# Kernel tuning notes

Measured on AMD Instinct MI355X. Metric: run time of the kernel, lower is better.

The kernel has to match this reference:

```python
import jax, jax.numpy as jnp
import numpy as np

B, C, S, HID = 64, 512, 28, 256  # batch, channels, spatial size, LSTM hidden


def _param(k, shape):
    return jax.random.normal(k, shape, jnp.float32) * 0.05


def setup_inputs() -> dict:
    key = jax.random.key(0)
    ks = jax.random.split(key, 19)
    inp = {"x": jax.random.normal(ks[0], (B, C, S, S), jnp.float32)}
    # vertical bidirectional LSTM (input C, hidden HID), torch gate order i,f,g,o
    inp["v_wih_f"] = _param(ks[1], (4 * HID, C))
    inp["v_whh_f"] = _param(ks[2], (4 * HID, HID))
    inp["v_b_f"] = _param(ks[3], (4 * HID,))
    inp["v_wih_b"] = _param(ks[4], (4 * HID, C))
    inp["v_whh_b"] = _param(ks[5], (4 * HID, HID))
    inp["v_b_b"] = _param(ks[6], (4 * HID,))
    # horizontal bidirectional LSTM (input 2*HID=512, hidden HID)
    inp["h_wih_f"] = _param(ks[7], (4 * HID, 2 * HID))
    inp["h_whh_f"] = _param(ks[8], (4 * HID, HID))
    inp["h_b_f"] = _param(ks[9], (4 * HID,))
    inp["h_wih_b"] = _param(ks[10], (4 * HID, 2 * HID))
    inp["h_whh_b"] = _param(ks[11], (4 * HID, HID))
    inp["h_b_b"] = _param(ks[12], (4 * HID,))
    # 1x1 conv 512 -> 100 (10x10 attention kernel logits)
    inp["conv_w"] = _param(ks[13], (100, 2 * HID))
    inp["conv_b"] = _param(ks[14], (100,))
    return inp


def _lstm_scan(xs, wih, whh, b):
    # xs: [T, N, D] -> h sequence [T, N, HID]
    hdim = whh.shape[1]
    def step(carry, xt):
        h, c = carry
        gates = xt @ wih.T + h @ whh.T + b  # [N, 4H]
        i, f, g, o = jnp.split(gates, 4, axis=-1)
        c = jax.nn.sigmoid(f) * c + jax.nn.sigmoid(i) * jnp.tanh(g)
        h = jax.nn.sigmoid(o) * jnp.tanh(c)
        return (h, c), h
    n = xs.shape[1]
    z = jnp.zeros((n, hdim), xs.dtype)
    _, hs = jax.lax.scan(step, (z, z), xs)
    return hs


def _bilstm(x, wf, uf, bf, wb, ub, bb):
    # x: [N, T, D] -> [N, T, 2*HID]
    xs = jnp.swapaxes(x, 0, 1)
    hf = _lstm_scan(xs, wf, uf, bf)
    hb = _lstm_scan(xs[::-1], wb, ub, bb)[::-1]
    return jnp.swapaxes(jnp.concatenate([hf, hb], axis=-1), 0, 1)


def reference(x, v_wih_f, v_whh_f, v_b_f, v_wih_b, v_whh_b, v_b_b,
              h_wih_f, h_whh_f, h_b_f, h_wih_b, h_whh_b, h_b_b,
              conv_w, conv_b):
    b, c, s, _ = x.shape
    xt = jnp.transpose(x, (0, 3, 2, 1))            # [B, W, H, C]
    # vertical LSTM: seq over W, batched over (B, H)
    v_in = jnp.transpose(xt, (0, 2, 1, 3)).reshape(b * s, s, c)
    v_out = _bilstm(v_in, v_wih_f, v_whh_f, v_b_f, v_wih_b, v_whh_b, v_b_b)
    v_out = jnp.transpose(v_out.reshape(b, s, s, 2 * HID), (0, 2, 1, 3))  # [B, W, H, 512]
    # horizontal LSTM: seq over H, batched over (B, W)
    h_in = v_out.reshape(b * s, s, 2 * HID)
    h_out = _bilstm(h_in, h_wih_f, h_whh_f, h_b_f, h_wih_b, h_whh_b, h_b_b)
    feat = jnp.transpose(h_out.reshape(b, s, s, 2 * HID), (0, 3, 2, 1))  # [B, 512, H, W]
    # 1x1 conv -> [B, 100, H, W], softmax over 100 kernel entries
    kern = jnp.einsum('bfhw,of->bohw', feat, conv_w) + conv_b[None, :, None, None]
    kern = jax.nn.softmax(kern, axis=1)
    # faithful to torch: C-order reshape [B,100,H,W] -> (B*H*W, 100) kernels
    w = kern.reshape(b, s * s, 100)
    # grouped dilated conv3d == weighted sum over dilation-3 sampled 10x10 grid
    x_s = x[:, :, ::3, ::3].reshape(b, c, 100)     # [B, C, 100]
    out = jnp.einsum('bpk,bck->bpc', w, x_s)       # [B, H*W, C]
    return out.reshape(b, c, s, s)                 # faithful C-order reshape
```

## Files before the change

kernel.cpp:

```cpp
#include <hip/hip_runtime.h>
#include <hip/hip_bf16.h>
#include <stdint.h>

typedef __hip_bfloat16 bf16_t;
typedef __attribute__((ext_vector_type(8))) short short8;
typedef __attribute__((ext_vector_type(4))) float f32x4;
typedef __attribute__((ext_vector_type(4))) unsigned int u32x4;
typedef unsigned long long ull;

#define MFMA16(a, b, c) __builtin_amdgcn_mfma_f32_16x16x32_bf16(a, b, c, 0, 0, 0)

#define NROW 50176
#define NBATCH 1792

__device__ __forceinline__ void g2l16(const void* g, void* l) {
  __builtin_amdgcn_global_load_lds(
      (const __attribute__((address_space(1))) unsigned int*)g,
      (__attribute__((address_space(3))) unsigned int*)l, 16, 0, 0);
}
__device__ __forceinline__ float sigm(float x) { return 1.0f / (1.0f + __expf(-x)); }
__device__ __forceinline__ float tanh_(float x) { return 2.0f / (1.0f + __expf(-2.0f * x)) - 1.0f; }
__device__ __forceinline__ void stc(bf16_t* p, float v) { *p = __float2bfloat16(v); }
__device__ __forceinline__ void stc(float* p, float v) { *p = v; }
__device__ __forceinline__ float bf2f(unsigned short u) {
  return __uint_as_float((unsigned int)u << 16);
}

struct CvtArgs {
  const float* src[8];
  bf16_t* dst[8];
  int n[8];
};
__global__ void cvt_all(CvtArgs a) {
  int arr = blockIdx.y;
  int i = blockIdx.x * 256 + threadIdx.x;
  if (i < a.n[arr]) a.dst[arr][i] = __float2bfloat16(a.src[arr][i]);
}

__global__ void transpose_x(const float* __restrict__ x, bf16_t* __restrict__ Xin,
                            bf16_t* __restrict__ xs) {
  int c0 = blockIdx.x * 128, h = blockIdx.y, b = blockIdx.z;
  __shared__ __align__(16) short tile[128 * 29];
  const float* xb = x + ((size_t)b * 512 + c0) * 784 + h * 28;
  for (int e = threadIdx.x; e < 128 * 28; e += 256) {
    int cc = e / 28, w = e - cc * 28;
    tile[cc * 29 + w] = __bfloat16_as_short(__float2bfloat16(xb[(size_t)cc * 784 + w]));
  }
  __syncthreads();
  size_t orow0 = (size_t)(b * 28 + h) * 28;
  short* os = (short*)Xin;
  for (int e = threadIdx.x; e < 28 * 128; e += 256) {
    int w = e >> 7, cc = e & 127;
    int c = c0 + cc;
    os[(size_t)(c >> 5) * NROW * 32 + (orow0 + w) * 32 + (c & 31)] = tile[cc * 29 + w];
  }
  short* xss = (short*)xs;
  if (h % 3 == 0) {
    int kh = h / 3;
    for (int e = threadIdx.x; e < 1280; e += 256) {
      int cc = e / 10, kw = e - cc * 10;
      xss[((size_t)(b * 512) + c0 + cc) * 128 + kh * 10 + kw] = tile[cc * 29 + 3 * kw];
    }
  }
  if (h == 0) {
    for (int e = threadIdx.x; e < 128 * 28; e += 256) {
      int cc = e / 28, kp = e - cc * 28;
      xss[((size_t)(b * 512) + c0 + cc) * 128 + 100 + kp] = 0;
    }
  }
}

__global__ void pad_conv(const float* __restrict__ cw, const float* __restrict__ cb,
                         bf16_t* __restrict__ cwp, float* __restrict__ cbp,
                         unsigned int* __restrict__ bar) {
  int r = blockIdx.x;
  if (r == 0)
    for (int i = threadIdx.x; i < 7168; i += 128) bar[i] = 0;
  for (int i = threadIdx.x; i < 512; i += 128)
    cwp[r * 512 + i] = __float2bfloat16((r < 100) ? cw[r * 512 + i] : 0.0f);
  if (r == 0) cbp[threadIdx.x] = (threadIdx.x < 100) ? cb[threadIdx.x] : 0.0f;
}

template <typename CT, bool CPERM>
__global__ __launch_bounds__(256) void gemm_bt(
    const bf16_t* __restrict__ A, const bf16_t* __restrict__ B0,
    const bf16_t* __restrict__ B1, const float* __restrict__ bias0,
    const float* __restrict__ bias1, CT* __restrict__ C, int M, int N, int K) {
  __shared__ __align__(16) short As[2][128 * 32];
  __shared__ __align__(16) short Bs[2][128 * 32];
  int tid = threadIdx.x;
  int L = blockIdx.x;
  int xc = L & 7, j = L >> 3;
  int mp = xc * 49 + (j % 49);
  int nb = j / 49;
  int bm0 = mp * 128, bn0 = nb * 128;
  int lrow = tid >> 2, lseg = tid & 3;
  const char* Ag = (const char*)A + ((size_t)(bm0 + lrow) * 32 + lseg * 8) * 2;
  size_t Aadv = (size_t)M * 64;
  const float* biasp;
  const char *Bg1, *Bg2;
  int js = 0;
  if (CPERM) {
    int dir = nb >> 3;
    js = nb & 7;
    const bf16_t* Bsel = dir ? B1 : B0;
    biasp = dir ? bias1 : bias0;
    int br1 = (lrow >> 5) * 256 + js * 32 + (lrow & 31);
    int br2 = ((lrow + 64) >> 5) * 256 + js * 32 + (lrow & 31);
    Bg1 = (const char*)(Bsel + (size_t)br1 * K) + lseg * 16;
    Bg2 = (const char*)(Bsel + (size_t)br2 * K) + lseg * 16;
  } else {
    biasp = bias0 + bn0;
    Bg1 = (const char*)(B0 + (size_t)(bn0 + lrow) * K) + lseg * 16;
    Bg2 = Bg1 + (size_t)64 * K * 2;
  }
  int w = tid >> 6, l = tid & 63, lm = l & 15, lq = l >> 4;
  int wm = w & 1, wn = w >> 1;
  f32x4 acc[4][4] = {};
  for (int k0 = 0; k0 < K; k0 += 64) {
#pragma unroll
    for (int p = 0; p < 2; p++) {
      g2l16(Ag, (char*)As[p] + tid * 16);
      g2l16(Ag + 4096, (char*)As[p] + 4096 + tid * 16);
      g2l16(Bg1, (char*)Bs[p] + tid * 16);
      g2l16(Bg2, (char*)Bs[p] + 4096 + tid * 16);
      Ag += Aadv; Bg1 += 64; Bg2 += 64;
    }
    __syncthreads();
#pragma unroll
    for (int p = 0; p < 2; p++) {
      short8 afr[4], bfr[4];
#pragma unroll
      for (int i = 0; i < 4; i++) {
        afr[i] = *(const short8*)&As[p][(wm * 64 + i * 16 + lm) * 32 + lq * 8];
        bfr[i] = *(const short8*)&Bs[p][(wn * 64 + i * 16 + lm) * 32 + lq * 8];
      }
#pragma unroll
      for (int mi = 0; mi < 4; mi++)
#pragma unroll
        for (int ni = 0; ni < 4; ni++) acc[mi][ni] = MFMA16(afr[mi], bfr[ni], acc[mi][ni]);
    }
    __syncthreads();
  }
  float bv[4];
#pragma unroll
  for (int ni = 0; ni < 4; ni++) {
    int cb = wn * 64 + ni * 16 + lm;
    bv[ni] = CPERM ? biasp[(cb >> 5) * 256 + js * 32 + (cb & 31)] : biasp[cb];
  }
#pragma unroll
  for (int mi = 0; mi < 4; mi++)
#pragma unroll
    for (int ni = 0; ni < 4; ni++) {
      int col = bn0 + wn * 64 + ni * 16 + lm;
#pragma unroll
      for (int r = 0; r < 4; r++) {
        size_t row = bm0 + wm * 64 + mi * 16 + lq * 4 + r;
        stc(&C[row * N + col], acc[mi][ni][r] + bv[ni]);
      }
    }
}

__global__ __launch_bounds__(256) void conv_softmax(
    const bf16_t* __restrict__ A, const bf16_t* __restrict__ B0,
    const float* __restrict__ bias, bf16_t* __restrict__ Wscr, int M, int K) {
  __shared__ __align__(16) short As[2][128 * 32];
  __shared__ __align__(16) short Bs[2][128 * 32];
  __shared__ float part[2][128];
  int tid = threadIdx.x;
  int bm0 = blockIdx.x * 128;
  int lrow = tid >> 2, lseg = tid & 3;
  const char* Ag = (const char*)A + ((size_t)(bm0 + lrow) * 32 + lseg * 8) * 2;
  size_t Aadv = (size_t)M * 64;
  const char* Bg1 = (const char*)(B0 + (size_t)lrow * K) + lseg * 16;
  const char* Bg2 = Bg1 + (size_t)64 * K * 2;
  int w = tid >> 6, l = tid & 63, lm = l & 15, lq = l >> 4;
  int wm = w & 1, wn = w >> 1;
  f32x4 acc[4][4] = {};
  for (int k0 = 0; k0 < K; k0 += 64) {
#pragma unroll
    for (int p = 0; p < 2; p++) {
      g2l16(Ag, (char*)As[p] + tid * 16);
      g2l16(Ag + 4096, (char*)As[p] + 4096 + tid * 16);
      g2l16(Bg1, (char*)Bs[p] + tid * 16);
      g2l16(Bg2, (char*)Bs[p] + 4096 + tid * 16);
      Ag += Aadv; Bg1 += 64; Bg2 += 64;
    }
    __syncthreads();
#pragma unroll
    for (int p = 0; p < 2; p++) {
      short8 afr[4], bfr[4];
#pragma unroll
      for (int i = 0; i < 4; i++) {
        afr[i] = *(const short8*)&As[p][(wm * 64 + i * 16 + lm) * 32 + lq * 8];
        bfr[i] = *(const short8*)&Bs[p][(wn * 64 + i * 16 + lm) * 32 + lq * 8];
      }
#pragma unroll
      for (int mi = 0; mi < 4; mi++)
#pragma unroll
        for (int ni = 0; ni < 4; ni++) acc[mi][ni] = MFMA16(afr[mi], bfr[ni], acc[mi][ni]);
    }
    __syncthreads();
  }
  float bv[4];
  bool vld[4];
#pragma unroll
  for (int ni = 0; ni < 4; ni++) {
    int col = wn * 64 + ni * 16 + lm;
    bv[ni] = bias[col];
    vld[ni] = (col < 100);
  }
  float pmax[4][4];
#pragma unroll
  for (int mi = 0; mi < 4; mi++)
#pragma unroll
    for (int r = 0; r < 4; r++) {
      float m = -1e30f;
#pragma unroll
      for (int ni = 0; ni < 4; ni++)
        if (vld[ni]) m = fmaxf(m, acc[mi][ni][r] + bv[ni]);
      pmax[mi][r] = m;
    }
#pragma unroll
  for (int mask = 1; mask <= 8; mask <<= 1)
#pragma unroll
    for (int mi = 0; mi < 4; mi++)
#pragma unroll
      for (int r = 0; r < 4; r++) pmax[mi][r] = fmaxf(pmax[mi][r], __shfl_xor(pmax[mi][r], mask));
  if (lm == 0)
#pragma unroll
    for (int mi = 0; mi < 4; mi++)
#pragma unroll
      for (int r = 0; r < 4; r++) part[wn][wm * 64 + mi * 16 + lq * 4 + r] = pmax[mi][r];
  __syncthreads();
  float fm[4][4];
#pragma unroll
  for (int mi = 0; mi < 4; mi++)
#pragma unroll
    for (int r = 0; r < 4; r++)
      fm[mi][r] = fmaxf(pmax[mi][r], part[wn ^ 1][wm * 64 + mi * 16 + lq * 4 + r]);
  __syncthreads();
  float ev[4][4][4];
  float ps[4][4];
#pragma unroll
  for (int mi = 0; mi < 4; mi++)
#pragma unroll
    for (int r = 0; r < 4; r++) {
      float s = 0.0f;
#pragma unroll
      for (int ni = 0; ni < 4; ni++) {
        float e = vld[ni] ? __expf(acc[mi][ni][r] + bv[ni] - fm[mi][r]) : 0.0f;
        ev[mi][ni][r] = e;
        s += e;
      }
      ps[mi][r] = s;
    }
#pragma unroll
  for (int mask = 1; mask <= 8; mask <<= 1)
#pragma unroll
    for (int mi = 0; mi < 4; mi++)
#pragma unroll
      for (int r = 0; r < 4; r++) ps[mi][r] += __shfl_xor(ps[mi][r], mask);
  if (lm == 0)
#pragma unroll
    for (int mi = 0; mi < 4; mi++)
#pragma unroll
      for (int r = 0; r < 4; r++) part[wn][wm * 64 + mi * 16 + lq * 4 + r] = ps[mi][r];
  __syncthreads();
#pragma unroll
  for (int mi = 0; mi < 4; mi++)
#pragma unroll
    for (int r = 0; r < 4; r++) {
      float inv =
          1.0f / (ps[mi][r] + part[wn ^ 1][wm * 64 + mi * 16 + lq * 4 + r]);
      int grow = bm0 + wm * 64 + mi * 16 + lq * 4 + r;
      int b = grow / 784, q = grow - b * 784;
      size_t base = (size_t)b * 784 * 128;
#pragma unroll
      for (int ni = 0; ni < 4; ni++) {
        int col = wn * 64 + ni * 16 + lm;
        if (col < 100) {
          int mm = col * 784 + q;
          Wscr[base + (size_t)(mm / 100) * 128 + (mm % 100)] =
              __float2bfloat16(ev[mi][ni][r] * inv);
        }
      }
    }
}

__global__ __launch_bounds__(256, 2) void lstm_scan(
    const bf16_t* __restrict__ G, const bf16_t* __restrict__ whh_f,
    const bf16_t* __restrict__ whh_b, bf16_t* __restrict__ hA,
    bf16_t* __restrict__ hB, bf16_t* __restrict__ outb,
    unsigned int* __restrict__ bar) {
  int dir = blockIdx.y;
  int js = blockIdx.x & 7;
  int rg = blockIdx.x >> 3;
  int tid = threadIdx.x, w = tid >> 6, l = tid & 63, lm = l & 15, lq = l >> 4;
  const short* whh = (const short*)(dir ? whh_b : whh_f);
  __shared__ __align__(16) short Ws[128 * 256];
  __shared__ __align__(16) short ht[64 * 40];
#pragma unroll
  for (int i = 0; i < 16; i++) {
    int segid = i * 256 + tid;
    int row = segid >> 5, seg = segid & 31;
    int gate = row >> 5, jj = row & 31;
    short8 v = *(const short8*)&whh[((size_t)(gate * 256 + js * 32 + jj)) * 256 + seg * 8];
    *(short8*)&Ws[row * 256 + ((seg ^ (row & 7)) * 8)] = v;
  }
  __syncthreads();
  unsigned int* cnt = bar + (((dir * 28 + rg) << 2) + w) * 16;
  int r0 = rg * 64 + w * 16;
  size_t dbase = (size_t)dir * 458752;
  const unsigned short* Gb = (const unsigned short*)G + (size_t)dir * 1024 + js * 128;
  float creg[2][4] = {};
  unsigned short gvs[2][4][4];
  auto load_gvs = [&](int tt) {
#pragma unroll
    for (int nj = 0; nj < 2; nj++)
#pragma unroll
      for (int r = 0; r < 4; r++) {
        int bi = r0 + lq * 4 + r;
        const unsigned short* gp = Gb + ((size_t)bi * 28 + tt) * 2048 + nj * 16 + lm;
#pragma unroll
        for (int gate = 0; gate < 4; gate++) gvs[nj][gate][r] = gp[gate * 32];
      }
  };
  load_gvs(dir ? 27 : 0);
  int srow = w * 16 + (l >> 2), sseg = l & 3;
  int sbi = rg * 64 + srow;
  int sbb = sbi / 28, srr = sbi - sbb * 28;
#pragma unroll 1
  for (int s = 0; s < 28; s++) {
    int t = dir ? 27 - s : s;
    f32x4 acc[4][2] = {};
    if (s > 0) {
      unsigned int tgt = 8u * (unsigned)s;
      while (__hip_atomic_load(cnt, __ATOMIC_RELAXED, __HIP_MEMORY_SCOPE_AGENT) < tgt)
        __builtin_amdgcn_s_sleep(1);
      const ull* hrp = (const ull*)((s & 1) ? hA : hB);
      ull hq[8][2];
#pragma unroll
      for (int kk = 0; kk < 8; kk++) {
        size_t off = dbase + (size_t)kk * 57344 + (size_t)(r0 + lm) * 32 + lq * 8;
        hq[kk][0] =
            __hip_atomic_load(hrp + (off >> 2), __ATOMIC_RELAXED, __HIP_MEMORY_SCOPE_AGENT);
        hq[kk][1] = __hip_atomic_load(hrp + (off >> 2) + 1, __ATOMIC_RELAXED,
                                      __HIP_MEMORY_SCOPE_AGENT);
      }
#pragma unroll
      for (int kk = 0; kk < 8; kk++) {
        short8 a;
        ((ull*)&a)[0] = hq[kk][0];
        ((ull*)&a)[1] = hq[kk][1];
        int bseg = ((kk * 4 + lq) ^ (lm & 7)) * 8;
#pragma unroll
        for (int gate = 0; gate < 4; gate++)
#pragma unroll
          for (int nj = 0; nj < 2; nj++) {
            short8 b = *(const short8*)&Ws[(gate * 32 + nj * 16 + lm) * 256 + bseg];
            acc[gate][nj] = MFMA16(a, b, acc[gate][nj]);
          }
      }
    }
#pragma unroll
    for (int nj = 0; nj < 2; nj++)
#pragma unroll
      for (int r = 0; r < 4; r++) {
        float gi = bf2f(gvs[nj][0][r]) + acc[0][nj][r];
        float gf = bf2f(gvs[nj][1][r]) + acc[1][nj][r];
        float gg = bf2f(gvs[nj][2][r]) + acc[2][nj][r];
        float go = bf2f(gvs[nj][3][r]) + acc[3][nj][r];
        float cn = sigm(gf) * creg[nj][r] + sigm(gi) * tanh_(gg);
        float hn = sigm(go) * tanh_(cn);
        creg[nj][r] = cn;
        ht[(w * 16 + lq * 4 + r) * 40 + nj * 16 + lm] =
            __bfloat16_as_short(__float2bfloat16(hn));
      }
    {
      u32x4 v = *(const u32x4*)&ht[srow * 40 + sseg * 8];
      ull* hwp = (ull*)((s & 1) ? hB : hA);
      size_t off = dbase + (size_t)js * 57344 + (size_t)sbi * 32 + sseg * 8;
      ull q0 = ((const ull*)&v)[0];
      ull q1 = ((const ull*)&v)[1];
      __hip_atomic_store(hwp + (off >> 2), q0, __ATOMIC_RELAXED, __HIP_MEMORY_SCOPE_AGENT);
      __hip_atomic_store(hwp + (off >> 2) + 1, q1, __ATOMIC_RELAXED,
                         __HIP_MEMORY_SCOPE_AGENT);
      short* ob = (short*)outb + (size_t)(dir * 8 + js) * NROW * 32;
      *(u32x4*)&ob[((size_t)sbb * 784 + (size_t)t * 28 + srr) * 32 + sseg * 8] = v;
    }
    if (s < 27) {
      asm volatile("s_waitcnt vmcnt(0)" ::: "memory");
      if (l == 0)
        __hip_atomic_fetch_add(cnt, 1u, __ATOMIC_RELAXED, __HIP_MEMORY_SCOPE_AGENT);
      load_gvs(dir ? 26 - s : s + 1);
    }
  }
}

__global__ __launch_bounds__(256) void final_gemm(const bf16_t* __restrict__ Wscr,
                                                  const bf16_t* __restrict__ xs,
                                                  float* __restrict__ outp) {
  int L = blockIdx.x;
  int xc = L & 7, j = L >> 3;
  int b = xc + 8 * (j / 28);
  int inner = j % 28;
  int m0 = (inner % 7) * 112, n0 = (inner / 7) * 128;
  int tid = threadIdx.x, w = tid >> 6, l = tid & 63, lm = l & 15, lq = l >> 4;
  const short* Ab = (const short*)Wscr + (size_t)b * 784 * 128;
  const short* Bb = (const short*)xs + (size_t)b * 512 * 128;
  f32x4 acc[7][2] = {};
#pragma unroll
  for (int kk = 0; kk < 4; kk++) {
    short8 b0 = *(const short8*)&Bb[(size_t)(n0 + w * 32 + lm) * 128 + kk * 32 + lq * 8];
    short8 b1 = *(const short8*)&Bb[(size_t)(n0 + w * 32 + 16 + lm) * 128 + kk * 32 + lq * 8];
#pragma unroll
    for (int mi = 0; mi < 7; mi++) {
      short8 a = *(const short8*)&Ab[(size_t)(m0 + mi * 16 + lm) * 128 + kk * 32 + lq * 8];
      acc[mi][0] = MFMA16(a, b0, acc[mi][0]);
      acc[mi][1] = MFMA16(a, b1, acc[mi][1]);
    }
  }
#pragma unroll
  for (int mi = 0; mi < 7; mi++)
#pragma unroll
    for (int ni = 0; ni < 2; ni++) {
      int c = n0 + w * 32 + ni * 16 + lm;
#pragma unroll
      for (int r = 0; r < 4; r++) {
        int p = m0 + mi * 16 + lq * 4 + r;
        outp[(size_t)b * 401408 + (size_t)p * 512 + c] = acc[mi][ni][r];
      }
    }
}

extern "C" void kernel_launch(void* const* d_in, const int* in_sizes, int n_in,
                              void* d_out, int out_size, void* d_ws, size_t ws_size,
                              hipStream_t stream) {
  const float* x = (const float*)d_in[0];
  const float* v_wih_f = (const float*)d_in[1];
  const float* v_whh_f = (const float*)d_in[2];
  const float* v_b_f = (const float*)d_in[3];
  const float* v_wih_b = (const float*)d_in[4];
  const float* v_whh_b = (const float*)d_in[5];
  const float* v_b_b = (const float*)d_in[6];
  const float* h_wih_f = (const float*)d_in[7];
  const float* h_whh_f = (const float*)d_in[8];
  const float* h_b_f = (const float*)d_in[9];
  const float* h_wih_b = (const float*)d_in[10];
  const float* h_whh_b = (const float*)d_in[11];
  const float* h_b_b = (const float*)d_in[12];
  const float* conv_w = (const float*)d_in[13];
  const float* conv_b = (const float*)d_in[14];

  char* ws = (char*)d_ws;
  bf16_t* Xin = (bf16_t*)(ws);
  bf16_t* Vout = (bf16_t*)(ws + 51380224);
  bf16_t* G = (bf16_t*)(ws + 102760448);
  bf16_t* Wscr = (bf16_t*)(ws + 128450560);
  bf16_t* xs = (bf16_t*)(ws + 308281344);
  bf16_t* cwp = (bf16_t*)(ws + 316669952);
  float* cbp = (float*)(ws + 316801024);
  bf16_t* hstate = (bf16_t*)(ws + 316801536);
  unsigned int* bar = (unsigned int*)(ws + 318636544);
  bf16_t* wvf = (bf16_t*)(ws + 322306560);
  bf16_t* wvb = (bf16_t*)(ws + 323355136);
  bf16_t* uvf = (bf16_t*)(ws + 324403712);
  bf16_t* uvb = (bf16_t*)(ws + 324928000);
  bf16_t* whf = (bf16_t*)(ws + 325452288);
  bf16_t* whb = (bf16_t*)(ws + 326500864);
  bf16_t* uhf = (bf16_t*)(ws + 327549440);
  bf16_t* uhb = (bf16_t*)(ws + 328073728);
  bf16_t* Hout = Xin;

  CvtArgs ca;
  ca.src[0] = v_wih_f; ca.dst[0] = wvf; ca.n[0] = 524288;
  ca.src[1] = v_wih_b; ca.dst[1] = wvb; ca.n[1] = 524288;
  ca.src[2] = v_whh_f; ca.dst[2] = uvf; ca.n[2] = 262144;
  ca.src[3] = v_whh_b; ca.dst[3] = uvb; ca.n[3] = 262144;
  ca.src[4] = h_wih_f; ca.dst[4] = whf; ca.n[4] = 524288;
  ca.src[5] = h_wih_b; ca.dst[5] = whb; ca.n[5] = 524288;
  ca.src[6] = h_whh_f; ca.dst[6] = uhf; ca.n[6] = 262144;
  ca.src[7] = h_whh_b; ca.dst[7] = uhb; ca.n[7] = 262144;
  cvt_all<<<dim3(2048, 8), 256, 0, stream>>>(ca);

  transpose_x<<<dim3(4, 28, 64), 256, 0, stream>>>(x, Xin, xs);
  pad_conv<<<dim3(128), 128, 0, stream>>>(conv_w, conv_b, cwp, cbp, bar);

  gemm_bt<bf16_t, true><<<dim3(6272), 256, 0, stream>>>(
      Xin, wvf, wvb, v_b_f, v_b_b, G, NROW, 2048, 512);
  lstm_scan<<<dim3(224, 2), 256, 0, stream>>>(G, uvf, uvb, hstate, Xin, Vout, bar);

  gemm_bt<bf16_t, true><<<dim3(6272), 256, 0, stream>>>(
      Vout, whf, whb, h_b_f, h_b_b, G, NROW, 2048, 512);
  lstm_scan<<<dim3(224, 2), 256, 0, stream>>>(G, uhf, uhb, hstate, Vout, Hout, bar + 3584);

  conv_softmax<<<dim3(392), 256, 0, stream>>>(Hout, cwp, cbp, Wscr, NROW, 512);
  final_gemm<<<dim3(1792), 256, 0, stream>>>(Wscr, xs, (float*)d_out);
}
```

Baseline: 969.8 us.

## Replace input-projection GEMM with 256x256-tile, 4-stage pipelined, swizzled-LDS kernel

Replaces the 128x128 double-buffered input-projection GEMM with a 512-thread kernel using 256x256 tiles and a 4-deep ring of LDS stages. Loads are issued three stages ahead with explicit vmcnt waits and one barrier per k-step. A XOR swizzle on LDS rows avoids bank conflicts, and the gate-permuted column mapping is kept. The aim is to raise data reuse per tile and overlap global loads with MFMA work. In exchange it uses 128KB of LDS per block, more registers for the accumulators, and fewer blocks (1568).

```diff
diff --git a/kernel.cpp b/kernel.cpp
--- a/kernel.cpp
+++ b/kernel.cpp
@@ -20,8 +20,6 @@
 }
 __device__ __forceinline__ float sigm(float x) { return 1.0f / (1.0f + __expf(-x)); }
 __device__ __forceinline__ float tanh_(float x) { return 2.0f / (1.0f + __expf(-2.0f * x)) - 1.0f; }
-__device__ __forceinline__ void stc(bf16_t* p, float v) { *p = __float2bfloat16(v); }
-__device__ __forceinline__ void stc(float* p, float v) { *p = v; }
 __device__ __forceinline__ float bf2f(unsigned short u) {
   return __uint_as_float((unsigned int)u << 16);
 }
@@ -81,82 +79,106 @@
   if (r == 0) cbp[threadIdx.x] = (threadIdx.x < 100) ? cb[threadIdx.x] : 0.0f;
 }
 
-template <typename CT, bool CPERM>
-__global__ __launch_bounds__(256) void gemm_bt(
+__global__ __launch_bounds__(512, 2) void gemm256(
     const bf16_t* __restrict__ A, const bf16_t* __restrict__ B0,
     const bf16_t* __restrict__ B1, const float* __restrict__ bias0,
-    const float* __restrict__ bias1, CT* __restrict__ C, int M, int N, int K) {
-  __shared__ __align__(16) short As[2][128 * 32];
-  __shared__ __align__(16) short Bs[2][128 * 32];
+    const float* __restrict__ bias1, bf16_t* __restrict__ C, int M) {
+  __shared__ __align__(16) short Asl[4][256 * 32];
+  __shared__ __align__(16) short Bsl[4][256 * 32];
   int tid = threadIdx.x;
-  int L = blockIdx.x;
-  int xc = L & 7, j = L >> 3;
-  int mp = xc * 49 + (j % 49);
-  int nb = j / 49;
-  int bm0 = mp * 128, bn0 = nb * 128;
-  int lrow = tid >> 2, lseg = tid & 3;
-  const char* Ag = (const char*)A + ((size_t)(bm0 + lrow) * 32 + lseg * 8) * 2;
+  int w = tid >> 6, l = tid & 63, lm = l & 15, lq = l >> 4;
+  int wm = w >> 2, wn = w & 3;
+  int bm0 = blockIdx.x * 256, bn0 = blockIdx.y * 256;
+  const char* ag[2];
+  const char* bg[2];
+#pragma unroll
+  for (int s = 0; s < 2; s++) {
+    int i = s * 512 + tid;
+    int row = i >> 2, sl = i & 3;
+    int sg = sl ^ ((row ^ (row >> 2)) & 3);
+    ag[s] = (const char*)A + ((size_t)(bm0 + row) * 32 + sg * 8) * 2;
+    int pc = bn0 + row;
+    int dir = pc >> 10, wc = pc & 1023;
+    int js = wc >> 7, loc = wc & 127;
+    int brow = (loc >> 5) * 256 + js * 32 + (loc & 31);
+    const bf16_t* Bsel = dir ? B1 : B0;
+    bg[s] = (const char*)(Bsel + (size_t)brow * 512) + sg * 16;
+  }
   size_t Aadv = (size_t)M * 64;
-  const float* biasp;
-  const char *Bg1, *Bg2;
-  int js = 0;
-  if (CPERM) {
-    int dir = nb >> 3;
-    js = nb & 7;
-    const bf16_t* Bsel = dir ? B1 : B0;
-    biasp = dir ? bias1 : bias0;
-    int br1 = (lrow >> 5) * 256 + js * 32 + (lrow & 31);
-    int br2 = ((lrow + 64) >> 5) * 256 + js * 32 + (lrow & 31);
-    Bg1 = (const char*)(Bsel + (size_t)br1 * K) + lseg * 16;
-    Bg2 = (const char*)(Bsel + (size_t)br2 * K) + lseg * 16;
-  } else {
-    biasp = bias0 + bn0;
-    Bg1 = (const char*)(B0 + (size_t)(bn0 + lrow) * K) + lseg * 16;
-    Bg2 = Bg1 + (size_t)64 * K * 2;
-  }
-  int w = tid >> 6, l = tid & 63, lm = l & 15, lq = l >> 4;
-  int wm = w & 1, wn = w >> 1;
-  f32x4 acc[4][4] = {};
-  for (int k0 = 0; k0 < K; k0 += 64) {
-#pragma unroll
-    for (int p = 0; p < 2; p++) {
-      g2l16(Ag, (char*)As[p] + tid * 16);
-      g2l16(Ag + 4096, (char*)As[p] + 4096 + tid * 16);
-      g2l16(Bg1, (char*)Bs[p] + tid * 16);
-      g2l16(Bg2, (char*)Bs[p] + 4096 + tid * 16);
-      Ag += Aadv; Bg1 += 64; Bg2 += 64;
-    }
-    __syncthreads();
-#pragma unroll
-    for (int p = 0; p < 2; p++) {
-      short8 afr[4], bfr[4];
-#pragma unroll
-      for (int i = 0; i < 4; i++) {
-        afr[i] = *(const short8*)&As[p][(wm * 64 + i * 16 + lm) * 32 + lq * 8];
-        bfr[i] = *(const short8*)&Bs[p][(wn * 64 + i * 16 + lm) * 32 + lq * 8];
-      }
-#pragma unroll
-      for (int mi = 0; mi < 4; mi++)
-#pragma unroll
-        for (int ni = 0; ni < 4; ni++) acc[mi][ni] = MFMA16(afr[mi], bfr[ni], acc[mi][ni]);
-    }
-    __syncthreads();
+  auto stage = [&](int t) {
+    int s4 = t & 3;
+#pragma unroll
+    for (int s = 0; s < 2; s++)
+      g2l16(ag[s] + (size_t)t * Aadv, (char*)&Asl[s4][0] + (s * 512 + w * 64) * 16);
+#pragma unroll
+    for (int s = 0; s < 2; s++)
+      g2l16(bg[s] + (size_t)t * 64, (char*)&Bsl[s4][0] + (s * 512 + w * 64) * 16);
+  };
+  int aoff[8], boff[4];
+#pragma unroll
+  for (int mi = 0; mi < 8; mi++) {
+    int row = wm * 128 + mi * 16 + lm;
+    aoff[mi] = (row * 4 + (lq ^ ((row ^ (row >> 2)) & 3))) * 8;
+  }
+#pragma unroll
+  for (int ni = 0; ni < 4; ni++) {
+    int row = wn * 64 + ni * 16 + lm;
+    boff[ni] = (row * 4 + (lq ^ ((row ^ (row >> 2)) & 3))) * 8;
+  }
+  f32x4 acc[8][4] = {};
+  stage(0);
+  stage(1);
+  stage(2);
+  asm volatile("s_waitcnt vmcnt(8)" ::: "memory");
+  __builtin_amdgcn_sched_barrier(0);
+  __builtin_amdgcn_s_barrier();
+  __builtin_amdgcn_sched_barrier(0);
+#pragma unroll 1
+  for (int t = 0; t < 16; t++) {
+    if (t < 13) stage(t + 3);
+    int s4 = t & 3;
+    const short* Ab = &Asl[s4][0];
+    const short* Bb = &Bsl[s4][0];
+    short8 bfr[4];
+#pragma unroll
+    for (int ni = 0; ni < 4; ni++) bfr[ni] = *(const short8*)&Bb[boff[ni]];
+    __builtin_amdgcn_s_setprio(1);
+#pragma unroll
+    for (int mi = 0; mi < 8; mi++) {
+      short8 afr = *(const short8*)&Ab[aoff[mi]];
+#pragma unroll
+      for (int ni = 0; ni < 4; ni++) acc[mi][ni] = MFMA16(afr, bfr[ni], acc[mi][ni]);
+    }
+    __builtin_amdgcn_s_setprio(0);
+    if (t < 13)
+      asm volatile("s_waitcnt vmcnt(8)" ::: "memory");
+    else if (t == 13)
+      asm volatile("s_waitcnt vmcnt(4)" ::: "memory");
+    else if (t == 14)
+      asm volatile("s_waitcnt vmcnt(0)" ::: "memory");
+    if (t < 15) {
+      __builtin_amdgcn_sched_barrier(0);
+      __builtin_amdgcn_s_barrier();
+      __builtin_amdgcn_sched_barrier(0);
+    }
   }
   float bv[4];
 #pragma unroll
   for (int ni = 0; ni < 4; ni++) {
-    int cb = wn * 64 + ni * 16 + lm;
-    bv[ni] = CPERM ? biasp[(cb >> 5) * 256 + js * 32 + (cb & 31)] : biasp[cb];
-  }
-#pragma unroll
-  for (int mi = 0; mi < 4; mi++)
+    int pc = bn0 + wn * 64 + ni * 16 + lm;
+    int dir = pc >> 10, wc = pc & 1023;
+    const float* bp = dir ? bias1 : bias0;
+    bv[ni] = bp[((wc & 127) >> 5) * 256 + (wc >> 7) * 32 + (wc & 31)];
+  }
+#pragma unroll
+  for (int mi = 0; mi < 8; mi++)
 #pragma unroll
     for (int ni = 0; ni < 4; ni++) {
       int col = bn0 + wn * 64 + ni * 16 + lm;
 #pragma unroll
       for (int r = 0; r < 4; r++) {
-        size_t row = bm0 + wm * 64 + mi * 16 + lq * 4 + r;
-        stc(&C[row * N + col], acc[mi][ni][r] + bv[ni]);
+        size_t row = bm0 + wm * 128 + mi * 16 + lq * 4 + r;
+        C[row * 2048 + col] = __float2bfloat16(acc[mi][ni][r] + bv[ni]);
       }
     }
 }
@@ -487,12 +509,10 @@
   transpose_x<<<dim3(4, 28, 64), 256, 0, stream>>>(x, Xin, xs);
   pad_conv<<<dim3(128), 128, 0, stream>>>(conv_w, conv_b, cwp, cbp, bar);
 
-  gemm_bt<bf16_t, true><<<dim3(6272), 256, 0, stream>>>(
-      Xin, wvf, wvb, v_b_f, v_b_b, G, NROW, 2048, 512);
+  gemm256<<<dim3(196, 8), 512, 0, stream>>>(Xin, wvf, wvb, v_b_f, v_b_b, G, NROW);
   lstm_scan<<<dim3(224, 2), 256, 0, stream>>>(G, uvf, uvb, hstate, Xin, Vout, bar);
 
-  gemm_bt<bf16_t, true><<<dim3(6272), 256, 0, stream>>>(
-      Vout, whf, whb, h_b_f, h_b_b, G, NROW, 2048, 512);
+  gemm256<<<dim3(196, 8), 512, 0, stream>>>(Vout, whf, whb, h_b_f, h_b_b, G, NROW);
   lstm_scan<<<dim3(224, 2), 256, 0, stream>>>(G, uhf, uhb, hstate, Vout, Hout, bar + 3584);
 
   conv_softmax<<<dim3(392), 256, 0, stream>>>(Hout, cwp, cbp, Wscr, NROW, 512);
```

New measurement: 993.5 us. +2.4%, slower.
